# Kernel optimization log

Hardware: AMD Instinct MI355X
Metric: run time of the kernel (lower is better)

The kernel has to match this reference:

```python
import math
import jax, jax.numpy as jnp
import numpy as np

B, T, D = 8, 2048, 1024

def _gelu(x):
    # tanh-approx GELU, matching the torch module's _gelu
    c = math.sqrt(2.0 / math.pi)
    return 0.5 * x * (1.0 + jnp.tanh(c * (x + 0.044715 * x * x * x)))

def _normalize(x, axis):
    # matches F.normalize(eps=1e-12)
    n = jnp.linalg.norm(x, axis=axis, keepdims=True)
    return x / jnp.maximum(n, 1e-12)

def setup_inputs() -> dict:
    key = jax.random.key(0)
    k1, k2 = jax.random.split(key)
    x = jax.random.normal(k1, (B, T, D), dtype=jnp.float32)
    ema_out = _normalize(jax.random.normal(k2, (D,), dtype=jnp.float32), 0)[..., 0] if False else None
    ema = jax.random.normal(k2, (D,), dtype=jnp.float32)
    ema = ema / jnp.maximum(jnp.linalg.norm(ema), 1e-12)
    return {
        "x": x,
        "ema_out": ema,
        "logit_decay": jnp.float32(math.log(0.9 / 0.1)),
        "log_tau": jnp.float32(math.log(2.0)),
        "log_blend": jnp.float32(math.log(0.3 / 0.7)),
        "logit_blend_seq": jnp.float32(0.0),
    }

def reference(x, ema_out, logit_decay, log_tau, log_blend, logit_blend_seq):
    Bx, Tx, Dx = x.shape
    tau = jnp.exp(log_tau)
    alpha = jax.nn.sigmoid(log_blend)
    w_seq = jax.nn.sigmoid(logit_blend_seq)

    out = _gelu(x)                              # [B,T,D]
    out_norm = _normalize(out, -1)              # [B,T,D]
    ema_norm = ema_out / jnp.maximum(jnp.linalg.norm(ema_out), 1e-12)  # [D]

    ema_sim = jnp.einsum('btd,d->bt', out_norm, ema_norm)             # [B,T]
    sim_mat = jnp.einsum('btd,bsd->bts', out_norm, out_norm)          # [B,T,T]

    causal = jnp.tril(jnp.ones((Tx, Tx), dtype=bool), k=-1)           # strict past
    sim_past = jnp.where(causal[None], sim_mat, -2.0)
    seq_sim = jnp.max(sim_past, axis=-1)                              # [B,T]

    has_past = (jnp.arange(Tx) > 0)[None, :]                          # [1,T]
    seq_sim = jnp.where(has_past, seq_sim, ema_sim)

    familiarity = w_seq * seq_sim + (1.0 - w_seq) * ema_sim
    novelty = jnp.exp(-tau * familiarity)
    gate = 1.0 - alpha + alpha * novelty                              # [B,T]
    return out * gate[..., None]
```

## Files before the change

### kernel.cpp

```cpp
#include <hip/hip_runtime.h>
#include <math.h>

#define NB 8
#define TT 2048
#define DD 1024
#define NTI 16
#define NPAIR 136

typedef __attribute__((ext_vector_type(8))) short short8;
typedef __attribute__((ext_vector_type(4))) float floatx4;

__device__ inline unsigned short f2bf(float f) {
    unsigned u = __builtin_bit_cast(unsigned, f);
    unsigned r = (u + 0x7fffu + ((u >> 16) & 1u)) >> 16;
    return (unsigned short)r;
}

__device__ inline float bf2f(unsigned short u) {
    return __builtin_bit_cast(float, (unsigned)u << 16);
}

__device__ inline float fast_gelu(float x) {
    float z = 0.7978845608028654f * (x + 0.044715f * x * x * x);
    float e = __expf(2.0f * z);
    float th = 1.0f - 2.0f / (e + 1.0f);
    return 0.5f * x * (1.0f + th);
}

__global__ __launch_bounds__(256) void k_gelu_norm(
        const float* __restrict__ x, const float* __restrict__ ema,
        unsigned short* __restrict__ onrm, float* __restrict__ norms,
        float* __restrict__ ema_sim) {
    int row = blockIdx.x * 4 + (threadIdx.x >> 6);
    int lane = threadIdx.x & 63;
    const float4* xr = reinterpret_cast<const float4*>(x + (size_t)row * DD);
    const float4* er = reinterpret_cast<const float4*>(ema);
    float g[16];
    float ss = 0.f, dt = 0.f, e2 = 0.f;
#pragma unroll
    for (int j = 0; j < 4; ++j) {
        float4 v = xr[j * 64 + lane];
        float4 e = er[j * 64 + lane];
        float vv[4] = {v.x, v.y, v.z, v.w};
        float ee[4] = {e.x, e.y, e.z, e.w};
        e2 += ee[0] * ee[0] + ee[1] * ee[1] + ee[2] * ee[2] + ee[3] * ee[3];
#pragma unroll
        for (int i = 0; i < 4; ++i) {
            float o = fast_gelu(vv[i]);
            g[j * 4 + i] = o;
            ss += o * o;
            dt += o * ee[i];
        }
    }
#pragma unroll
    for (int m = 1; m < 64; m <<= 1) {
        ss += __shfl_xor(ss, m);
        dt += __shfl_xor(dt, m);
        e2 += __shfl_xor(e2, m);
    }
    float nrm = fmaxf(sqrtf(ss), 1e-12f);
    float inv = 1.0f / nrm;
    float einv = 1.0f / fmaxf(sqrtf(e2), 1e-12f);
    ushort4* orow = reinterpret_cast<ushort4*>(onrm + (size_t)row * DD);
#pragma unroll
    for (int j = 0; j < 4; ++j) {
        ushort4 u;
        u.x = f2bf(g[j * 4 + 0] * inv);
        u.y = f2bf(g[j * 4 + 1] * inv);
        u.z = f2bf(g[j * 4 + 2] * inv);
        u.w = f2bf(g[j * 4 + 3] * inv);
        orow[j * 64 + lane] = u;
    }
    if (lane == 0) {
        norms[row] = nrm;
        ema_sim[row] = dt * inv * einv;
    }
}

__global__ void k_seqmax(const unsigned short* __restrict__ onrm,
                         float* __restrict__ part) {
    __shared__ unsigned short lds[2][8192];

    int id = blockIdx.x;
    int nid = (id & 7) * NPAIR + (id >> 3);
    int b = nid / NPAIR;
    int p = nid % NPAIR;
    int ti = (int)((sqrtf(8.0f * (float)p + 1.0f) - 1.0f) * 0.5f);
    while ((ti + 1) * (ti + 2) / 2 <= p) ++ti;
    while (ti * (ti + 1) / 2 > p) --ti;
    int sj = p - ti * (ti + 1) / 2;

    int lane = threadIdx.x & 63;
    int wave = threadIdx.x >> 6;
    int wr = wave >> 1, wc = wave & 1;

    const unsigned short* Abase = onrm + (size_t)(b * TT + ti * 128) * DD;
    const unsigned short* Bbase = onrm + (size_t)(b * TT + sj * 128) * DD;

    floatx4 acc[4][4];
#pragma unroll
    for (int i = 0; i < 4; i++)
#pragma unroll
        for (int j = 0; j < 4; j++) acc[i][j] = (floatx4){0.f, 0.f, 0.f, 0.f};

    auto stage = [&](int kt) {
#pragma unroll
        for (int i = 0; i < 4; ++i) {
            int c = wave * 4 + i;
            int off = c * 1024 + lane * 16;
            int row = off >> 7;
            int colb = (off & 127) ^ ((row & 7) << 4);
            const char* srcA = (const char*)(Abase + (size_t)row * DD + kt * 64) + colb;
            const char* srcB = (const char*)(Bbase + (size_t)row * DD + kt * 64) + colb;
            __builtin_amdgcn_global_load_lds(
                (const __attribute__((address_space(1))) unsigned int*)srcA,
                (__attribute__((address_space(3))) unsigned int*)((char*)&lds[0][0] + c * 1024),
                16, 0, 0);
            __builtin_amdgcn_global_load_lds(
                (const __attribute__((address_space(1))) unsigned int*)srcB,
                (__attribute__((address_space(3))) unsigned int*)((char*)&lds[1][0] + c * 1024),
                16, 0, 0);
        }
    };

    for (int kt = 0; kt < 16; ++kt) {
        stage(kt);
        __syncthreads();
        const char* Ab = (const char*)&lds[0][0];
        const char* Bb = (const char*)&lds[1][0];
#pragma unroll
        for (int ks = 0; ks < 2; ++ks) {
            short8 af[4], bg[4];
            int cb = ks * 64 + ((lane >> 4) << 4);
#pragma unroll
            for (int f = 0; f < 4; ++f) {
                int ar = wr * 64 + f * 16 + (lane & 15);
                int br = wc * 64 + f * 16 + (lane & 15);
                af[f] = *(const short8*)(Ab + ar * 128 + (cb ^ ((ar & 7) << 4)));
                bg[f] = *(const short8*)(Bb + br * 128 + (cb ^ ((br & 7) << 4)));
            }
#pragma unroll
            for (int fi = 0; fi < 4; ++fi)
#pragma unroll
                for (int fj = 0; fj < 4; ++fj)
                    acc[fi][fj] = __builtin_amdgcn_mfma_f32_16x16x32_bf16(
                        af[fi], bg[fj], acc[fi][fj], 0, 0, 0);
        }
        __syncthreads();
    }

    int g = lane >> 4;
    int t0g = ti * 128 + wr * 64;
    int s0g = sj * 128 + wc * 64;
#pragma unroll
    for (int fi = 0; fi < 4; ++fi) {
#pragma unroll
        for (int r = 0; r < 4; ++r) {
            int trow = t0g + fi * 16 + g * 4 + r;
            float m = -2.0f;
#pragma unroll
            for (int fj = 0; fj < 4; ++fj) {
                int scol = s0g + fj * 16 + (lane & 15);
                m = fmaxf(m, (scol < trow) ? acc[fi][fj][r] : -2.0f);
            }
#pragma unroll
            for (int msk = 1; msk < 16; msk <<= 1) m = fmaxf(m, __shfl_xor(m, msk));
            if ((lane & 15) == 0)
                part[(((size_t)b * 32 + sj * 2 + wc) << 11) + trow] = m;
        }
    }
}

__global__ __launch_bounds__(256) void k_gate(
        const unsigned short* __restrict__ onrm, const float* __restrict__ norms,
        float* __restrict__ out, const float* __restrict__ ema_sim,
        const float* __restrict__ part,
        const float* __restrict__ log_tau,
        const float* __restrict__ log_blend,
        const float* __restrict__ logit_blend_seq) {
    int row = blockIdx.x * 4 + (threadIdx.x >> 6);
    int lane = threadIdx.x & 63;
    int b = row >> 11;
    int t = row & (TT - 1);

    int n = 2 * ((t >> 7) + 1);
    float m = (lane < n) ? part[(((size_t)b * 32 + lane) << 11) + t] : -2.0f;
#pragma unroll
    for (int msk = 1; msk < 64; msk <<= 1) m = fmaxf(m, __shfl_xor(m, msk));

    float tau = __expf(log_tau[0]);
    float alpha = 1.f / (1.f + __expf(-log_blend[0]));
    float wseq = 1.f / (1.f + __expf(-logit_blend_seq[0]));
    float es = ema_sim[row];
    float sq = (t > 0) ? m : es;
    float fam = wseq * sq + (1.f - wseq) * es;
    float gate = 1.f - alpha + alpha * __expf(-tau * fam);
    float scale = gate * norms[row];

    const ushort4* ir = reinterpret_cast<const ushort4*>(onrm + (size_t)row * DD);
    float4* orow = reinterpret_cast<float4*>(out + (size_t)row * DD);
#pragma unroll
    for (int j = 0; j < 4; ++j) {
        ushort4 u = ir[j * 64 + lane];
        float4 o;
        o.x = bf2f(u.x) * scale;
        o.y = bf2f(u.y) * scale;
        o.z = bf2f(u.z) * scale;
        o.w = bf2f(u.w) * scale;
        orow[j * 64 + lane] = o;
    }
}

extern "C" void kernel_launch(void* const* d_in, const int* in_sizes, int n_in,
                              void* d_out, int out_size, void* d_ws, size_t ws_size,
                              hipStream_t stream) {
    const float* x = (const float*)d_in[0];
    const float* ema = (const float*)d_in[1];
    const float* log_tau = (const float*)d_in[3];
    const float* log_blend = (const float*)d_in[4];
    const float* logit_bs = (const float*)d_in[5];
    float* out = (float*)d_out;

    char* ws = (char*)d_ws;
    float* ema_sim = (float*)(ws + (4 << 10));
    float* norms = (float*)(ws + (68 << 10));
    float* part = (float*)(ws + (132 << 10));
    unsigned short* onrm = (unsigned short*)(ws + ((size_t)2304 << 10));

    k_gelu_norm<<<NB * TT / 4, 256, 0, stream>>>(x, ema, onrm, norms, ema_sim);
    k_seqmax<<<NB * NPAIR, 256, 0, stream>>>(onrm, part);
    k_gate<<<NB * TT / 4, 256, 0, stream>>>(onrm, norms, out, ema_sim, part,
                                            log_tau, log_blend, logit_bs);
}
```

Measured before the change: 87.10 us.

## Double-buffer LDS tiles in seqmax GEMM to overlap global loads with MFMA

The similarity-max kernel now uses two LDS buffers per operand and prefetches the next K tile with global_load_lds before computing on the current one. A manual vmcnt wait and raw s_barrier replace __syncthreads, and s_setprio is raised around the MFMA section. This aims to hide global-to-LDS latency behind matrix math, at the cost of doubling LDS use per block (64KB), which may lower occupancy.

```diff
diff --git a/kernel.cpp b/kernel.cpp
--- a/kernel.cpp
+++ b/kernel.cpp
@@ -79,7 +79,7 @@
 
 __global__ void k_seqmax(const unsigned short* __restrict__ onrm,
                          float* __restrict__ part) {
-    __shared__ unsigned short lds[2][8192];
+    __shared__ unsigned short lds[2][2][8192];
 
     int id = blockIdx.x;
     int nid = (id & 7) * NPAIR + (id >> 3);
@@ -103,7 +103,7 @@
 #pragma unroll
         for (int j = 0; j < 4; j++) acc[i][j] = (floatx4){0.f, 0.f, 0.f, 0.f};
 
-    auto stage = [&](int kt) {
+    auto stage = [&](int buf, int kt) {
 #pragma unroll
         for (int i = 0; i < 4; ++i) {
             int c = wave * 4 + i;
@@ -114,20 +114,31 @@
             const char* srcB = (const char*)(Bbase + (size_t)row * DD + kt * 64) + colb;
             __builtin_amdgcn_global_load_lds(
                 (const __attribute__((address_space(1))) unsigned int*)srcA,
-                (__attribute__((address_space(3))) unsigned int*)((char*)&lds[0][0] + c * 1024),
+                (__attribute__((address_space(3))) unsigned int*)((char*)&lds[buf][0][0] + c * 1024),
                 16, 0, 0);
             __builtin_amdgcn_global_load_lds(
                 (const __attribute__((address_space(1))) unsigned int*)srcB,
-                (__attribute__((address_space(3))) unsigned int*)((char*)&lds[1][0] + c * 1024),
+                (__attribute__((address_space(3))) unsigned int*)((char*)&lds[buf][1][0] + c * 1024),
                 16, 0, 0);
         }
     };
 
+    stage(0, 0);
+
+#pragma unroll
     for (int kt = 0; kt < 16; ++kt) {
-        stage(kt);
-        __syncthreads();
-        const char* Ab = (const char*)&lds[0][0];
-        const char* Bb = (const char*)&lds[1][0];
+        int buf = kt & 1;
+        if (kt + 1 < 16) {
+            stage(buf ^ 1, kt + 1);
+            asm volatile("s_waitcnt vmcnt(8)" ::: "memory");
+        } else {
+            asm volatile("s_waitcnt vmcnt(0)" ::: "memory");
+        }
+        __builtin_amdgcn_s_barrier();
+        __builtin_amdgcn_sched_barrier(0);
+        const char* Ab = (const char*)&lds[buf][0][0];
+        const char* Bb = (const char*)&lds[buf][1][0];
+        __builtin_amdgcn_s_setprio(1);
 #pragma unroll
         for (int ks = 0; ks < 2; ++ks) {
             short8 af[4], bg[4];
@@ -146,7 +157,9 @@
                     acc[fi][fj] = __builtin_amdgcn_mfma_f32_16x16x32_bf16(
                         af[fi], bg[fj], acc[fi][fj], 0, 0, 0);
         }
-        __syncthreads();
+        __builtin_amdgcn_s_setprio(0);
+        __builtin_amdgcn_sched_barrier(0);
+        __builtin_amdgcn_s_barrier();
     }
 
     int g = lane >> 4;
```

Measured after the change: 91.06 us. 4.5% more time.

## Load MFMA operands directly from global memory with register double-buffering

Applied to the files above, without the earlier changes.

The seqmax GEMM kernel stops staging A/B tiles through LDS with global_load_lds and barriers. Each wave now loads its bf16 fragments straight from global memory into registers, alternating two buffers so the next half-K loads can be issued while MFMAs run on the current ones. This removes LDS traffic and both __syncthreads per K step. In exchange, the two waves sharing a row or column block each fetch the same data from global/L2, and the loads are 16-byte pieces strided across rows, not cooperative coalesced tiles.

```diff
diff --git a/kernel.cpp b/kernel.cpp
--- a/kernel.cpp
+++ b/kernel.cpp
@@ -77,10 +77,8 @@
     }
 }
 
-__global__ void k_seqmax(const unsigned short* __restrict__ onrm,
-                         float* __restrict__ part) {
-    __shared__ unsigned short lds[2][8192];
-
+__global__ __launch_bounds__(256) void k_seqmax(const unsigned short* __restrict__ onrm,
+                                                float* __restrict__ part) {
     int id = blockIdx.x;
     int nid = (id & 7) * NPAIR + (id >> 3);
     int b = nid / NPAIR;
@@ -93,9 +91,12 @@
     int lane = threadIdx.x & 63;
     int wave = threadIdx.x >> 6;
     int wr = wave >> 1, wc = wave & 1;
-
-    const unsigned short* Abase = onrm + (size_t)(b * TT + ti * 128) * DD;
-    const unsigned short* Bbase = onrm + (size_t)(b * TT + sj * 128) * DD;
+    int rl = lane & 15, g = lane >> 4;
+
+    const unsigned short* Abp =
+        onrm + (size_t)(b * TT + ti * 128 + wr * 64 + rl) * DD + g * 8;
+    const unsigned short* Bbp =
+        onrm + (size_t)(b * TT + sj * 128 + wc * 64 + rl) * DD + g * 8;
 
     floatx4 acc[4][4];
 #pragma unroll
@@ -103,53 +104,31 @@
 #pragma unroll
         for (int j = 0; j < 4; j++) acc[i][j] = (floatx4){0.f, 0.f, 0.f, 0.f};
 
-    auto stage = [&](int kt) {
-#pragma unroll
-        for (int i = 0; i < 4; ++i) {
-            int c = wave * 4 + i;
-            int off = c * 1024 + lane * 16;
-            int row = off >> 7;
-            int colb = (off & 127) ^ ((row & 7) << 4);
-            const char* srcA = (const char*)(Abase + (size_t)row * DD + kt * 64) + colb;
-            const char* srcB = (const char*)(Bbase + (size_t)row * DD + kt * 64) + colb;
-            __builtin_amdgcn_global_load_lds(
-                (const __attribute__((address_space(1))) unsigned int*)srcA,
-                (__attribute__((address_space(3))) unsigned int*)((char*)&lds[0][0] + c * 1024),
-                16, 0, 0);
-            __builtin_amdgcn_global_load_lds(
-                (const __attribute__((address_space(1))) unsigned int*)srcB,
-                (__attribute__((address_space(3))) unsigned int*)((char*)&lds[1][0] + c * 1024),
-                16, 0, 0);
+    auto ld = [&](short8* da, short8* db, int off) {
+#pragma unroll
+        for (int f = 0; f < 4; ++f) {
+            da[f] = *(const short8*)(Abp + (size_t)f * 16 * DD + off);
+            db[f] = *(const short8*)(Bbp + (size_t)f * 16 * DD + off);
         }
     };
-
+    auto mm = [&](short8* a, short8* bfr) {
+#pragma unroll
+        for (int fi = 0; fi < 4; ++fi)
+#pragma unroll
+            for (int fj = 0; fj < 4; ++fj)
+                acc[fi][fj] = __builtin_amdgcn_mfma_f32_16x16x32_bf16(
+                    a[fi], bfr[fj], acc[fi][fj], 0, 0, 0);
+    };
+
+    short8 a0[4], b0[4], a1[4], b1[4];
+    ld(a0, b0, 0);
     for (int kt = 0; kt < 16; ++kt) {
-        stage(kt);
-        __syncthreads();
-        const char* Ab = (const char*)&lds[0][0];
-        const char* Bb = (const char*)&lds[1][0];
-#pragma unroll
-        for (int ks = 0; ks < 2; ++ks) {
-            short8 af[4], bg[4];
-            int cb = ks * 64 + ((lane >> 4) << 4);
-#pragma unroll
-            for (int f = 0; f < 4; ++f) {
-                int ar = wr * 64 + f * 16 + (lane & 15);
-                int br = wc * 64 + f * 16 + (lane & 15);
-                af[f] = *(const short8*)(Ab + ar * 128 + (cb ^ ((ar & 7) << 4)));
-                bg[f] = *(const short8*)(Bb + br * 128 + (cb ^ ((br & 7) << 4)));
-            }
-#pragma unroll
-            for (int fi = 0; fi < 4; ++fi)
-#pragma unroll
-                for (int fj = 0; fj < 4; ++fj)
-                    acc[fi][fj] = __builtin_amdgcn_mfma_f32_16x16x32_bf16(
-                        af[fi], bg[fj], acc[fi][fj], 0, 0, 0);
-        }
-        __syncthreads();
-    }
-
-    int g = lane >> 4;
+        ld(a1, b1, kt * 64 + 32);
+        mm(a0, b0);
+        if (kt + 1 < 16) ld(a0, b0, (kt + 1) * 64);
+        mm(a1, b1);
+    }
+
     int t0g = ti * 128 + wr * 64;
     int s0g = sj * 128 + wc * 64;
 #pragma unroll
@@ -160,12 +139,12 @@
             float m = -2.0f;
 #pragma unroll
             for (int fj = 0; fj < 4; ++fj) {
-                int scol = s0g + fj * 16 + (lane & 15);
+                int scol = s0g + fj * 16 + rl;
                 m = fmaxf(m, (scol < trow) ? acc[fi][fj][r] : -2.0f);
             }
 #pragma unroll
             for (int msk = 1; msk < 16; msk <<= 1) m = fmaxf(m, __shfl_xor(m, msk));
-            if ((lane & 15) == 0)
+            if (rl == 0)
                 part[(((size_t)b * 32 + sj * 2 + wc) << 11) + trow] = m;
         }
     }
```

Measured after the change: 190.5 us. 119% more time.

## Quantize normalized activations to FP8 and use scaled FP8 MFMA for similarity

Applied to the files above, without the earlier changes.

The normalized GELU rows are now stored as FP8 (e4m3) instead of bf16, and the causal similarity GEMM uses the 16x16x128 scaled f8f6f4 MFMA. This halves the intermediate traffic and the MFMA instruction count. The gate kernel now recomputes GELU from the original fp32 input rather than rescaling the stored bf16 copy, which also drops the norms buffer. The cost is lower precision in the similarity max, which may shift gate values beyond tolerance, and an extra GELU evaluation in the final pass.

```diff
diff --git a/kernel.cpp b/kernel.cpp
--- a/kernel.cpp
+++ b/kernel.cpp
@@ -7,18 +7,9 @@
 #define NTI 16
 #define NPAIR 136
 
-typedef __attribute__((ext_vector_type(8))) short short8;
+typedef __attribute__((ext_vector_type(4))) int intx4;
+typedef __attribute__((ext_vector_type(8))) int intx8;
 typedef __attribute__((ext_vector_type(4))) float floatx4;
-
-__device__ inline unsigned short f2bf(float f) {
-    unsigned u = __builtin_bit_cast(unsigned, f);
-    unsigned r = (u + 0x7fffu + ((u >> 16) & 1u)) >> 16;
-    return (unsigned short)r;
-}
-
-__device__ inline float bf2f(unsigned short u) {
-    return __builtin_bit_cast(float, (unsigned)u << 16);
-}
 
 __device__ inline float fast_gelu(float x) {
     float z = 0.7978845608028654f * (x + 0.044715f * x * x * x);
@@ -29,8 +20,7 @@
 
 __global__ __launch_bounds__(256) void k_gelu_norm(
         const float* __restrict__ x, const float* __restrict__ ema,
-        unsigned short* __restrict__ onrm, float* __restrict__ norms,
-        float* __restrict__ ema_sim) {
+        unsigned int* __restrict__ onrm8, float* __restrict__ ema_sim) {
     int row = blockIdx.x * 4 + (threadIdx.x >> 6);
     int lane = threadIdx.x & 63;
     const float4* xr = reinterpret_cast<const float4*>(x + (size_t)row * DD);
@@ -58,28 +48,22 @@
         dt += __shfl_xor(dt, m);
         e2 += __shfl_xor(e2, m);
     }
-    float nrm = fmaxf(sqrtf(ss), 1e-12f);
-    float inv = 1.0f / nrm;
+    float inv = 1.0f / fmaxf(sqrtf(ss), 1e-12f);
     float einv = 1.0f / fmaxf(sqrtf(e2), 1e-12f);
-    ushort4* orow = reinterpret_cast<ushort4*>(onrm + (size_t)row * DD);
+    unsigned int* o8 = onrm8 + (size_t)row * (DD / 4);
 #pragma unroll
     for (int j = 0; j < 4; ++j) {
-        ushort4 u;
-        u.x = f2bf(g[j * 4 + 0] * inv);
-        u.y = f2bf(g[j * 4 + 1] * inv);
-        u.z = f2bf(g[j * 4 + 2] * inv);
-        u.w = f2bf(g[j * 4 + 3] * inv);
-        orow[j * 64 + lane] = u;
-    }
-    if (lane == 0) {
-        norms[row] = nrm;
-        ema_sim[row] = dt * inv * einv;
-    }
-}
-
-__global__ void k_seqmax(const unsigned short* __restrict__ onrm,
+        int pk = 0;
+        pk = __builtin_amdgcn_cvt_pk_fp8_f32(g[j * 4 + 0] * inv, g[j * 4 + 1] * inv, pk, false);
+        pk = __builtin_amdgcn_cvt_pk_fp8_f32(g[j * 4 + 2] * inv, g[j * 4 + 3] * inv, pk, true);
+        o8[j * 64 + lane] = (unsigned int)pk;
+    }
+    if (lane == 0) ema_sim[row] = dt * inv * einv;
+}
+
+__global__ void k_seqmax(const unsigned char* __restrict__ onrm8,
                          float* __restrict__ part) {
-    __shared__ unsigned short lds[2][8192];
+    __shared__ unsigned char lds[32768];
 
     int id = blockIdx.x;
     int nid = (id & 7) * NPAIR + (id >> 3);
@@ -93,9 +77,10 @@
     int lane = threadIdx.x & 63;
     int wave = threadIdx.x >> 6;
     int wr = wave >> 1, wc = wave & 1;
-
-    const unsigned short* Abase = onrm + (size_t)(b * TT + ti * 128) * DD;
-    const unsigned short* Bbase = onrm + (size_t)(b * TT + sj * 128) * DD;
+    int rl = lane & 15, g = lane >> 4;
+
+    const unsigned char* Abase = onrm8 + (size_t)(b * TT + ti * 128) * DD;
+    const unsigned char* Bbase = onrm8 + (size_t)(b * TT + sj * 128) * DD;
 
     floatx4 acc[4][4];
 #pragma unroll
@@ -110,46 +95,45 @@
             int off = c * 1024 + lane * 16;
             int row = off >> 7;
             int colb = (off & 127) ^ ((row & 7) << 4);
-            const char* srcA = (const char*)(Abase + (size_t)row * DD + kt * 64) + colb;
-            const char* srcB = (const char*)(Bbase + (size_t)row * DD + kt * 64) + colb;
+            const unsigned char* srcA = Abase + (size_t)row * DD + kt * 128 + colb;
+            const unsigned char* srcB = Bbase + (size_t)row * DD + kt * 128 + colb;
             __builtin_amdgcn_global_load_lds(
                 (const __attribute__((address_space(1))) unsigned int*)srcA,
-                (__attribute__((address_space(3))) unsigned int*)((char*)&lds[0][0] + c * 1024),
+                (__attribute__((address_space(3))) unsigned int*)(&lds[0] + c * 1024),
                 16, 0, 0);
             __builtin_amdgcn_global_load_lds(
                 (const __attribute__((address_space(1))) unsigned int*)srcB,
-                (__attribute__((address_space(3))) unsigned int*)((char*)&lds[1][0] + c * 1024),
+                (__attribute__((address_space(3))) unsigned int*)(&lds[16384] + c * 1024),
                 16, 0, 0);
         }
     };
 
-    for (int kt = 0; kt < 16; ++kt) {
+    int g2 = g * 2;
+    auto ldfrag = [&](const unsigned char* base, int r) -> intx8 {
+        int sw = (r & 7) << 4;
+        intx4 lo = *(const intx4*)(base + r * 128 + ((g2 * 16) ^ sw));
+        intx4 hi = *(const intx4*)(base + r * 128 + ((g2 * 16 + 16) ^ sw));
+        return __builtin_shufflevector(lo, hi, 0, 1, 2, 3, 4, 5, 6, 7);
+    };
+
+    for (int kt = 0; kt < 8; ++kt) {
         stage(kt);
         __syncthreads();
-        const char* Ab = (const char*)&lds[0][0];
-        const char* Bb = (const char*)&lds[1][0];
-#pragma unroll
-        for (int ks = 0; ks < 2; ++ks) {
-            short8 af[4], bg[4];
-            int cb = ks * 64 + ((lane >> 4) << 4);
-#pragma unroll
-            for (int f = 0; f < 4; ++f) {
-                int ar = wr * 64 + f * 16 + (lane & 15);
-                int br = wc * 64 + f * 16 + (lane & 15);
-                af[f] = *(const short8*)(Ab + ar * 128 + (cb ^ ((ar & 7) << 4)));
-                bg[f] = *(const short8*)(Bb + br * 128 + (cb ^ ((br & 7) << 4)));
-            }
-#pragma unroll
-            for (int fi = 0; fi < 4; ++fi)
-#pragma unroll
-                for (int fj = 0; fj < 4; ++fj)
-                    acc[fi][fj] = __builtin_amdgcn_mfma_f32_16x16x32_bf16(
-                        af[fi], bg[fj], acc[fi][fj], 0, 0, 0);
-        }
+        intx8 af[4], bg[4];
+#pragma unroll
+        for (int f = 0; f < 4; ++f) {
+            af[f] = ldfrag(&lds[0], wr * 64 + f * 16 + rl);
+            bg[f] = ldfrag(&lds[16384], wc * 64 + f * 16 + rl);
+        }
+#pragma unroll
+        for (int fi = 0; fi < 4; ++fi)
+#pragma unroll
+            for (int fj = 0; fj < 4; ++fj)
+                acc[fi][fj] = __builtin_amdgcn_mfma_scale_f32_16x16x128_f8f6f4(
+                    af[fi], bg[fj], acc[fi][fj], 0, 0, 0, 127, 0, 127);
         __syncthreads();
     }
 
-    int g = lane >> 4;
     int t0g = ti * 128 + wr * 64;
     int s0g = sj * 128 + wc * 64;
 #pragma unroll
@@ -160,21 +144,20 @@
             float m = -2.0f;
 #pragma unroll
             for (int fj = 0; fj < 4; ++fj) {
-                int scol = s0g + fj * 16 + (lane & 15);
+                int scol = s0g + fj * 16 + rl;
                 m = fmaxf(m, (scol < trow) ? acc[fi][fj][r] : -2.0f);
             }
 #pragma unroll
             for (int msk = 1; msk < 16; msk <<= 1) m = fmaxf(m, __shfl_xor(m, msk));
-            if ((lane & 15) == 0)
+            if (rl == 0)
                 part[(((size_t)b * 32 + sj * 2 + wc) << 11) + trow] = m;
         }
     }
 }
 
 __global__ __launch_bounds__(256) void k_gate(
-        const unsigned short* __restrict__ onrm, const float* __restrict__ norms,
-        float* __restrict__ out, const float* __restrict__ ema_sim,
-        const float* __restrict__ part,
+        const float* __restrict__ x, float* __restrict__ out,
+        const float* __restrict__ ema_sim, const float* __restrict__ part,
         const float* __restrict__ log_tau,
         const float* __restrict__ log_blend,
         const float* __restrict__ logit_blend_seq) {
@@ -195,18 +178,17 @@
     float sq = (t > 0) ? m : es;
     float fam = wseq * sq + (1.f - wseq) * es;
     float gate = 1.f - alpha + alpha * __expf(-tau * fam);
-    float scale = gate * norms[row];
-
-    const ushort4* ir = reinterpret_cast<const ushort4*>(onrm + (size_t)row * DD);
+
+    const float4* xr = reinterpret_cast<const float4*>(x + (size_t)row * DD);
     float4* orow = reinterpret_cast<float4*>(out + (size_t)row * DD);
 #pragma unroll
     for (int j = 0; j < 4; ++j) {
-        ushort4 u = ir[j * 64 + lane];
+        float4 v = xr[j * 64 + lane];
         float4 o;
-        o.x = bf2f(u.x) * scale;
-        o.y = bf2f(u.y) * scale;
-        o.z = bf2f(u.z) * scale;
-        o.w = bf2f(u.w) * scale;
+        o.x = fast_gelu(v.x) * gate;
+        o.y = fast_gelu(v.y) * gate;
+        o.z = fast_gelu(v.z) * gate;
+        o.w = fast_gelu(v.w) * gate;
         orow[j * 64 + lane] = o;
     }
 }
@@ -223,12 +205,11 @@
 
     char* ws = (char*)d_ws;
     float* ema_sim = (float*)(ws + (4 << 10));
-    float* norms = (float*)(ws + (68 << 10));
     float* part = (float*)(ws + (132 << 10));
-    unsigned short* onrm = (unsigned short*)(ws + ((size_t)2304 << 10));
-
-    k_gelu_norm<<<NB * TT / 4, 256, 0, stream>>>(x, ema, onrm, norms, ema_sim);
-    k_seqmax<<<NB * NPAIR, 256, 0, stream>>>(onrm, part);
-    k_gate<<<NB * TT / 4, 256, 0, stream>>>(onrm, norms, out, ema_sim, part,
+    unsigned char* onrm8 = (unsigned char*)(ws + ((size_t)2304 << 10));
+
+    k_gelu_norm<<<NB * TT / 4, 256, 0, stream>>>(x, ema, (unsigned int*)onrm8, ema_sim);
+    k_seqmax<<<NB * NPAIR, 256, 0, stream>>>(onrm8, part);
+    k_gate<<<NB * TT / 4, 256, 0, stream>>>(x, out, ema_sim, part,
                                             log_tau, log_blend, logit_bs);
 }
```

New measurement: 301.7 us. +246.3%, slower.
